# Performance work log

Hardware: AMD Instinct MI355X
Metric: run time of the kernel (lower is better)

The kernel has to match this reference:

```python
import jax, jax.numpy as jnp
import numpy as np

NUM_GROUPS = 32
EPS = 1e-5


def group_norm(x, w, b):
    # x: [B, C, H, W]
    B, C, H, W = x.shape
    g = x.reshape(B, NUM_GROUPS, C // NUM_GROUPS, H, W)
    mu = g.mean(axis=(2, 3, 4), keepdims=True)
    var = g.var(axis=(2, 3, 4), keepdims=True)
    g = (g - mu) * jax.lax.rsqrt(var + EPS)
    x = g.reshape(B, C, H, W)
    return x * w[None, :, None, None] + b[None, :, None, None]


def conv1x1(x, w, b):
    # 1x1 conv == channel matmul; x: [B, C, H, W], w: [O, C], b: [O]
    return jnp.einsum('bchw,oc->bohw', x, w) + b[None, :, None, None]


def setup_inputs() -> dict:
    key = jax.random.key(0)
    ks = jax.random.split(key, 11)
    C = 512
    B, H, W = 4, 64, 64
    s = 1.0 / np.sqrt(C)
    return {
        'x': jax.random.normal(ks[0], (B, C, H, W), jnp.float32),
        'gn_w': jax.random.uniform(ks[1], (C,), jnp.float32, 0.5, 1.5),
        'gn_b': jax.random.normal(ks[2], (C,), jnp.float32) * 0.1,
        'wq': jax.random.normal(ks[3], (C, C), jnp.float32) * s,
        'bq': jax.random.normal(ks[4], (C,), jnp.float32) * 0.01,
        'wk': jax.random.normal(ks[5], (C, C), jnp.float32) * s,
        'bk': jax.random.normal(ks[6], (C,), jnp.float32) * 0.01,
        'wv': jax.random.normal(ks[7], (C, C), jnp.float32) * s,
        'bv': jax.random.normal(ks[8], (C,), jnp.float32) * 0.01,
        'wo': jax.random.normal(ks[9], (C, C), jnp.float32) * s,
        'bo': jax.random.normal(ks[10], (C,), jnp.float32) * 0.01,
    }


def reference(x, gn_w, gn_b, wq, bq, wk, bk, wv, bv, wo, bo):
    B, C, H, W = x.shape
    h_ = group_norm(x, gn_w, gn_b)
    q = conv1x1(h_, wq, bq).reshape(B, C, H * W)   # [B, C, HW]
    k = conv1x1(h_, wk, bk).reshape(B, C, H * W)
    v = conv1x1(h_, wv, bv).reshape(B, C, H * W)
    # scores: q^T k, scaled by C^-0.5; softmax over keys
    scores = jnp.einsum('bci,bcj->bij', q, k) * (C ** -0.5)  # [B, HW, HW]
    attn = jax.nn.softmax(scores, axis=-1)
    # h_[b,c,i] = sum_j v[b,c,j] * attn[b,i,j]
    h_ = jnp.einsum('bcj,bij->bci', v, attn).reshape(B, C, H, W)
    return x + conv1x1(h_, wo, bo)
```

## Files before the change

### kernel.cpp

```cpp
#include <hip/hip_runtime.h>
#include <hip/hip_bf16.h>

typedef __attribute__((ext_vector_type(8))) __bf16 bf16x8;
typedef __attribute__((ext_vector_type(4))) float f32x4;

__device__ __forceinline__ unsigned short f2bf(float f) {
  union { float f; unsigned u; } v; v.f = f;
  unsigned r = v.u + 0x7fffu + ((v.u >> 16) & 1u);
  return (unsigned short)(r >> 16);
}

__device__ __forceinline__ void gload_lds16(const void* g, void* s) {
  __builtin_amdgcn_global_load_lds(
      (const __attribute__((address_space(1))) void*)g,
      (__attribute__((address_space(3))) void*)s, 16, 0, 0);
}

__global__ __launch_bounds__(256) void convert_w(
    const float* __restrict__ wq, const float* __restrict__ wk,
    const float* __restrict__ wv, const float* __restrict__ wo,
    unsigned short* __restrict__ dst, float* __restrict__ lrow) {
  if (blockIdx.x >= 4096) {
    lrow[((blockIdx.x - 4096) << 8) | threadIdx.x] = 0.f;
    return;
  }
  const int m = blockIdx.x >> 10;
  const float* src = (m == 0) ? wq : (m == 1) ? wk : (m == 2) ? wv : wo;
  const int idx = ((blockIdx.x & 1023) << 8) | threadIdx.x;
  dst[m * 262144 + idx] = f2bf(src[idx]);
}

__global__ __launch_bounds__(256) void zero_k(float* __restrict__ p, int n) {
  const int i = blockIdx.x * 256 + threadIdx.x;
  if (i < n) p[i] = 0.f;
}

__global__ __launch_bounds__(256) void gn_stats(
    const float* __restrict__ x, float2* __restrict__ partials) {
  const int bg = blockIdx.x >> 2, part = blockIdx.x & 3;
  const float* xg = x + (size_t)bg * 65536 + part * 1024;
  const int t = threadIdx.x;
  float s = 0.f, ss = 0.f;
#pragma unroll
  for (int r = 0; r < 16; ++r) {
    const float4 v = *(const float4*)(xg + (size_t)r * 4096 + t * 4);
    s += v.x + v.y + v.z + v.w;
    ss += v.x * v.x + v.y * v.y + v.z * v.z + v.w * v.w;
  }
#pragma unroll
  for (int m = 32; m; m >>= 1) { s += __shfl_xor(s, m); ss += __shfl_xor(ss, m); }
  __shared__ float red[8];
  const int wave = t >> 6, lane = t & 63;
  if (lane == 0) { red[wave] = s; red[wave + 4] = ss; }
  __syncthreads();
  if (t == 0) {
    float2 p;
    p.x = red[0] + red[1] + red[2] + red[3];
    p.y = red[4] + red[5] + red[6] + red[7];
    partials[blockIdx.x] = p;
  }
}

__global__ __launch_bounds__(256) void gn_apply(
    const float* __restrict__ x, const float2* __restrict__ partials,
    const float* __restrict__ gw, const float* __restrict__ gb,
    unsigned short* __restrict__ h_t) {
  const int bg = blockIdx.x >> 3, cc = blockIdx.x & 7;
  const int b = bg >> 5, g = bg & 31;
  const int t = threadIdx.x;
  __shared__ float chs[32];
  __shared__ unsigned short tile[16][520];
  if (t < 16) {
    const float2 p0 = partials[bg * 4 + 0], p1 = partials[bg * 4 + 1];
    const float2 p2 = partials[bg * 4 + 2], p3 = partials[bg * 4 + 3];
    const float S = p0.x + p1.x + p2.x + p3.x;
    const float SS = p0.y + p1.y + p2.y + p3.y;
    const float mu = S * (1.f / 65536.f);
    const float rstd = rsqrtf(SS * (1.f / 65536.f) - mu * mu + 1e-5f);
    const float sc = gw[g * 16 + t] * rstd;
    chs[t] = sc;
    chs[16 + t] = gb[g * 16 + t] - mu * sc;
  }
  __syncthreads();
  const float* xg = x + (size_t)bg * 65536 + cc * 512;
#pragma unroll
  for (int rr = 0; rr < 8; ++rr) {
    const int r = rr * 2 + (t >> 7), i = (t & 127) * 4;
    const float4 v = *(const float4*)(xg + (size_t)r * 4096 + i);
    const float sc = chs[r], sh = chs[16 + r];
    ushort4 o;
    o.x = f2bf(v.x * sc + sh); o.y = f2bf(v.y * sc + sh);
    o.z = f2bf(v.z * sc + sh); o.w = f2bf(v.w * sc + sh);
    *(ushort4*)&tile[r][i] = o;
  }
  __syncthreads();
  unsigned short* outp = h_t + ((size_t)b * 4096 + cc * 512) * 512 + g * 16;
#pragma unroll
  for (int rep = 0; rep < 4; ++rep) {
    const int task = rep * 256 + t;
    const int nl = task >> 1, half = (task & 1) * 8;
    ushort4 o0, o1;
    o0.x = tile[half + 0][nl]; o0.y = tile[half + 1][nl];
    o0.z = tile[half + 2][nl]; o0.w = tile[half + 3][nl];
    o1.x = tile[half + 4][nl]; o1.y = tile[half + 5][nl];
    o1.z = tile[half + 6][nl]; o1.w = tile[half + 7][nl];
    *(ushort4*)(outp + (size_t)nl * 512 + half) = o0;
    *(ushort4*)(outp + (size_t)nl * 512 + half + 4) = o1;
  }
}

__global__ __launch_bounds__(256) void reduce4_k(
    const float* __restrict__ part, const float* __restrict__ l,
    unsigned short* __restrict__ dst) {
  const size_t i = ((size_t)blockIdx.x * 256 + threadIdx.x) * 4;
  f32x4 s0 = *(const f32x4*)(part + i);
  f32x4 s1 = *(const f32x4*)(part + 2097152 + i);
  f32x4 s2 = *(const f32x4*)(part + 4194304 + i);
  f32x4 s3 = *(const f32x4*)(part + 6291456 + i);
  f32x4 s = (s0 + s1) + (s2 + s3);
  const float inv = 1.f / l[i >> 9];
  ushort4 o;
  o.x = f2bf(s[0] * inv); o.y = f2bf(s[1] * inv);
  o.z = f2bf(s[2] * inv); o.w = f2bf(s[3] * inv);
  *(ushort4*)(dst + i) = o;
}

__global__ __launch_bounds__(256) void gemm_qkv(
    const unsigned short* __restrict__ H, const unsigned short* __restrict__ W,
    unsigned short* __restrict__ q_t, unsigned short* __restrict__ k_t,
    unsigned short* __restrict__ v_ct,
    const float* __restrict__ bq, const float* __restrict__ bk,
    const float* __restrict__ bv, float qscale) {
  __shared__ __align__(16) char smem[49152];
  const int tid = threadIdx.x;
  const int wave = tid >> 6, lane = tid & 63;
  const int l15 = lane & 15, l4 = lane >> 4;
  const int wm = wave >> 1, wn = wave & 1;

  const int bx = blockIdx.x, by = blockIdx.y, bz = blockIdx.z;
  const int mode = bx >> 2;
  const int colv = (bx & 3) << 7;
  const int row0 = by << 7;
  const unsigned short* A = H + (size_t)bz * 2097152;
  const unsigned short* Bt = W + (size_t)bx * 65536;

  const int ar = tid >> 2;
  const int akc = (tid & 3) ^ ((tid >> 3) & 3);

  auto stage = [&](int kt, int bi) {
    const int kb = kt << 5;
    char* sAl = smem + bi * 16384 + wave * 1024;
    char* sBl = sAl + 8192;
    const unsigned short* gA = A + (size_t)(row0 + ar) * 512 + kb + akc * 8;
    const unsigned short* gB = Bt + (size_t)ar * 512 + kb + akc * 8;
    gload_lds16(gA, sAl);
    gload_lds16(gB, sBl);
    gload_lds16(gA + (size_t)64 * 512, sAl + 4096);
    gload_lds16(gB + (size_t)64 * 512, sBl + 4096);
  };

  f32x4 acc[4][4];
#pragma unroll
  for (int r = 0; r < 4; ++r)
#pragma unroll
    for (int c = 0; c < 4; ++c) acc[r][c] = (f32x4)0.f;

  const int xsw = (l4 ^ ((l15 >> 1) & 3)) << 4;

  auto compute = [&](int bi) {
    const char* pa = smem + bi * 16384 + (wm * 64 + l15) * 64 + xsw;
    const char* pb = smem + bi * 16384 + 8192 + (wn * 64 + l15) * 64 + xsw;
    bf16x8 af[4], bfr[4];
#pragma unroll
    for (int r = 0; r < 4; ++r) af[r] = *(const bf16x8*)(pa + r * 1024);
#pragma unroll
    for (int c = 0; c < 4; ++c) bfr[c] = *(const bf16x8*)(pb + c * 1024);
#pragma unroll
    for (int r = 0; r < 4; ++r)
#pragma unroll
      for (int c = 0; c < 4; ++c)
        acc[r][c] = __builtin_amdgcn_mfma_f32_16x16x32_bf16(af[r], bfr[c], acc[r][c], 0, 0, 0);
  };

  stage(0, 0);
  stage(1, 1);
  int bi = 0;
  for (int kt = 0; kt < 15; ++kt) {
    asm volatile("s_waitcnt vmcnt(4)" ::: "memory");
    __builtin_amdgcn_s_barrier();
    __builtin_amdgcn_sched_barrier(0);
    if (kt + 2 < 16) stage(kt + 2, (kt + 2) % 3);
    compute(bi);
    bi = (bi == 2) ? 0 : bi + 1;
  }
  asm volatile("s_waitcnt vmcnt(0)" ::: "memory");
  __builtin_amdgcn_s_barrier();
  __builtin_amdgcn_sched_barrier(0);
  compute(bi);

  const float* bias = (mode == 0) ? bq : (mode == 1) ? bk : bv;
  const float scale = (mode == 0) ? qscale : 1.0f;
  __syncthreads();
  if (mode < 2) {
    unsigned short* outp = ((mode == 0) ? q_t : k_t) + (size_t)bz * 2097152;
    unsigned short* tile = (unsigned short*)smem;
#pragma unroll
    for (int c = 0; c < 4; ++c) {
      const int coll = wn * 64 + c * 16 + l15;
      const float badd = bias[colv + coll];
#pragma unroll
      for (int r = 0; r < 4; ++r) {
        const int rowl = wm * 64 + r * 16 + l4 * 4;
#pragma unroll
        for (int j = 0; j < 4; ++j)
          tile[(rowl + j) * 136 + coll] = f2bf((acc[r][c][j] + badd) * scale);
      }
    }
    __syncthreads();
#pragma unroll
    for (int it = 0; it < 8; ++it) {
      const int idx = it * 256 + tid;
      const int rw = idx >> 4, ch = (idx & 15) * 8;
      const uint4 vv = *(const uint4*)&tile[rw * 136 + ch];
      *(uint4*)(outp + (size_t)(row0 + rw) * 512 + colv + ch) = vv;
    }
  } else {
    unsigned short* outp = v_ct + (size_t)bz * 2097152;
    unsigned short* tile = (unsigned short*)smem;
#pragma unroll
    for (int c = 0; c < 4; ++c) {
      const int coll = wn * 64 + c * 16 + l15;
      const float badd = bias[colv + coll];
#pragma unroll
      for (int r = 0; r < 4; ++r) {
        const int rowl = wm * 64 + r * 16 + l4 * 4;
#pragma unroll
        for (int j = 0; j < 4; ++j)
          tile[(rowl + j) * 132 + coll] = f2bf(acc[r][c][j] + badd);
      }
    }
    __syncthreads();
#pragma unroll 8
    for (int it = 0; it < 64; ++it) {
      const int idx = it * 256 + tid;
      const int cl = idx >> 7, il = idx & 127;
      outp[(size_t)(colv + cl) * 4096 + row0 + il] = tile[il * 132 + cl];
    }
  }
}

__global__ __launch_bounds__(512, 4) void gemm_s256(
    const unsigned short* __restrict__ A, const unsigned short* __restrict__ Bt,
    unsigned short* __restrict__ Out, float* __restrict__ lsum) {
  __shared__ __align__(16) char smem[73728];
  const int tid = threadIdx.x;
  const int wave = tid >> 6, lane = tid & 63;
  const int l15 = lane & 15, l4 = lane >> 4;
  const int wm = wave >> 1, wn = wave & 1;

  const int bz = blockIdx.z;
  A += (size_t)bz * 2097152;
  Bt += (size_t)bz * 2097152;
  Out += (size_t)bz * 16777216;
  lsum += (size_t)bz * 4096;

  const int id = blockIdx.y * 32 + blockIdx.x;
  const int xcd = id & 7, j = id >> 3;
  const int by = ((xcd >> 1) << 2) + (j >> 4);
  const int bx = ((xcd & 1) << 4) + (j & 15);
  const int row0 = by << 8, col0 = bx << 7;

  const int ar = tid >> 2;
  const int akc = (tid & 3) ^ ((tid >> 3) & 3);

  auto stage = [&](int kt, int bi) {
    const int kb = kt << 5;
    char* base = smem + bi * 24576;
    const unsigned short* gA = A + (size_t)(row0 + ar) * 512 + kb + akc * 8;
    const unsigned short* gB = Bt + (size_t)(col0 + ar) * 512 + kb + akc * 8;
    gload_lds16(gA, base + wave * 1024);
    gload_lds16(gA + (size_t)128 * 512, base + 8192 + wave * 1024);
    gload_lds16(gB, base + 16384 + wave * 1024);
  };

  f32x4 acc[4][4];
#pragma unroll
  for (int r = 0; r < 4; ++r)
#pragma unroll
    for (int c = 0; c < 4; ++c) acc[r][c] = (f32x4)0.f;

  const int xsw = (l4 ^ ((l15 >> 1) & 3)) << 4;

  auto compute = [&](int bi) {
    const char* pa = smem + bi * 24576 + (wm * 64 + l15) * 64 + xsw;
    const char* pb = smem + bi * 24576 + 16384 + (wn * 64 + l15) * 64 + xsw;
    bf16x8 af[4], bfr[4];
#pragma unroll
    for (int r = 0; r < 4; ++r) af[r] = *(const bf16x8*)(pa + r * 1024);
#pragma unroll
    for (int c = 0; c < 4; ++c) bfr[c] = *(const bf16x8*)(pb + c * 1024);
#pragma unroll
    for (int r = 0; r < 4; ++r)
#pragma unroll
      for (int c = 0; c < 4; ++c)
        acc[r][c] = __builtin_amdgcn_mfma_f32_16x16x32_bf16(af[r], bfr[c], acc[r][c], 0, 0, 0);
  };

  stage(0, 0);
  stage(1, 1);
  int bi = 0;
  for (int kt = 0; kt < 15; ++kt) {
    asm volatile("s_waitcnt vmcnt(3)" ::: "memory");
    __builtin_amdgcn_s_barrier();
    __builtin_amdgcn_sched_barrier(0);
    if (kt + 2 < 16) stage(kt + 2, (kt + 2) % 3);
    compute(bi);
    bi = (bi == 2) ? 0 : bi + 1;
  }
  asm volatile("s_waitcnt vmcnt(0)" ::: "memory");
  __builtin_amdgcn_s_barrier();
  __builtin_amdgcn_sched_barrier(0);
  compute(bi);

  __syncthreads();
  unsigned short* tile = (unsigned short*)smem;
#pragma unroll
  for (int c = 0; c < 4; ++c) {
    const int coll = wn * 64 + c * 16 + l15;
#pragma unroll
    for (int r = 0; r < 4; ++r) {
      const int rowl = wm * 64 + r * 16 + l4 * 4;
#pragma unroll
      for (int j = 0; j < 4; ++j)
        tile[(rowl + j) * 136 + coll] = f2bf(__expf(acc[r][c][j]));
    }
  }
  __syncthreads();
#pragma unroll
  for (int it = 0; it < 8; ++it) {
    const int idx = it * 512 + tid;
    const int rw = idx >> 4, ch = (idx & 15) * 8;
    const uint4 vv = *(const uint4*)&tile[rw * 136 + ch];
    *(uint4*)(Out + (size_t)(row0 + rw) * 4096 + col0 + ch) = vv;
    const unsigned* uu = (const unsigned*)&vv;
    float s = 0.f;
#pragma unroll
    for (int q = 0; q < 4; ++q) {
      union { unsigned u; float f; } w;
      w.u = uu[q] << 16; s += w.f;
      w.u = uu[q] & 0xffff0000u; s += w.f;
    }
    s += __shfl_xor(s, 1); s += __shfl_xor(s, 2);
    s += __shfl_xor(s, 4); s += __shfl_xor(s, 8);
    if ((lane & 15) == 0) atomicAdd(&lsum[row0 + rw], s);
  }
}

__global__ __launch_bounds__(512, 2) void gemm_pv(
    const unsigned short* __restrict__ P, const unsigned short* __restrict__ Vt,
    unsigned short* __restrict__ Out, const float* __restrict__ lrow) {
  __shared__ __align__(16) char smem[147456];
  const int tid = threadIdx.x;
  const int wave = tid >> 6, lane = tid & 63;
  const int l15 = lane & 15, l4 = lane >> 4;
  const int wm = wave >> 1, wn = wave & 1;

  const int L = blockIdx.x + ((blockIdx.y + (blockIdx.z << 4)) << 2);
  const int xcd = L & 7, j = L >> 3;
  const int panel = xcd * 8 + (j >> 2);
  const int bx = j & 3, by = panel & 15, bz = panel >> 4;
  const int row0 = by << 8, col0 = bx << 7;
  P += (size_t)bz * 16777216;
  Vt += (size_t)bz * 2097152;
  Out += (size_t)bz * 2097152;
  lrow += bz * 4096;

  const int sr = tid >> 3;
  const int sc8 = (tid & 7) ^ (sr & 7);
  const unsigned short* gA = P + (size_t)(row0 + sr) * 4096 + sc8 * 8;
  const unsigned short* gB = Vt + (size_t)(col0 + sr) * 4096 + sc8 * 8;

  auto stA = [&](int kt, int bi, int p) {
    gload_lds16(gA + (size_t)(p << 6) * 4096 + (kt << 6),
                smem + bi * 49152 + p * 8192 + wave * 1024);
  };
  auto stB = [&](int kt, int bi, int p) {
    gload_lds16(gB + (size_t)(p << 6) * 4096 + (kt << 6),
                smem + bi * 49152 + 32768 + p * 8192 + wave * 1024);
  };

  f32x4 acc[4][4];
#pragma unroll
  for (int r = 0; r < 4; ++r)
#pragma unroll
    for (int c = 0; c < 4; ++c) acc[r][c] = (f32x4)0.f;

  const int sw0 = (l4 ^ (l15 & 7)) << 4;
  const int sw1 = ((4 + l4) ^ (l15 & 7)) << 4;
  const int arow = (wm * 64 + l15) << 7;
  const int brow = (wn * 64 + l15) << 7;

  bf16x8 bfr[4][2];

  stA(0, 0, 0); stA(0, 0, 1); stA(0, 0, 2); stA(0, 0, 3);
  stB(0, 0, 0); stB(0, 0, 1);
  stA(1, 1, 0); stA(1, 1, 1); stA(1, 1, 2); stA(1, 1, 3);
  stB(1, 1, 0); stB(1, 1, 1);
  asm volatile("s_waitcnt vmcnt(6)" ::: "memory");
  __builtin_amdgcn_s_barrier();
  __builtin_amdgcn_sched_barrier(0);

  int bi = 0;
#pragma unroll 1
  for (int kt = 0; kt < 64; ++kt) {
    const char* bufA = smem + bi * 49152;
    const char* bufB = bufA + 32768;
    const int pb = (bi + 2) % 3;
    const bool pre = (kt + 2 < 64);
    bf16x8 a0, a1;
    a0 = *(const bf16x8*)(bufA + arow + sw0);
    a1 = *(const bf16x8*)(bufA + arow + sw1);
#pragma unroll
    for (int c = 0; c < 4; ++c) {
      bfr[c][0] = *(const bf16x8*)(bufB + brow + c * 2048 + sw0);
      bfr[c][1] = *(const bf16x8*)(bufB + brow + c * 2048 + sw1);
    }
    if (pre) { stA(kt + 2, pb, 0); stA(kt + 2, pb, 1); }
    __builtin_amdgcn_s_barrier();
    asm volatile("s_waitcnt lgkmcnt(0)" ::: "memory");
    __builtin_amdgcn_sched_barrier(0);
    __builtin_amdgcn_s_setprio(1);
#pragma unroll
    for (int c = 0; c < 4; ++c) {
      acc[0][c] = __builtin_amdgcn_mfma_f32_16x16x32_bf16(a0, bfr[c][0], acc[0][c], 0, 0, 0);
      acc[0][c] = __builtin_amdgcn_mfma_f32_16x16x32_bf16(a1, bfr[c][1], acc[0][c], 0, 0, 0);
    }
    __builtin_amdgcn_s_setprio(0);
    __builtin_amdgcn_s_barrier();
    a0 = *(const bf16x8*)(bufA + arow + 2048 + sw0);
    a1 = *(const bf16x8*)(bufA + arow + 2048 + sw1);
    if (pre) { stA(kt + 2, pb, 2); stA(kt + 2, pb, 3); }
    __builtin_amdgcn_s_barrier();
    asm volatile("s_waitcnt lgkmcnt(0)" ::: "memory");
    __builtin_amdgcn_sched_barrier(0);
    __builtin_amdgcn_s_setprio(1);
#pragma unroll
    for (int c = 0; c < 4; ++c) {
      acc[1][c] = __builtin_amdgcn_mfma_f32_16x16x32_bf16(a0, bfr[c][0], acc[1][c], 0, 0, 0);
      acc[1][c] = __builtin_amdgcn_mfma_f32_16x16x32_bf16(a1, bfr[c][1], acc[1][c], 0, 0, 0);
    }
    __builtin_amdgcn_s_setprio(0);
    __builtin_amdgcn_s_barrier();
    a0 = *(const bf16x8*)(bufA + arow + 4096 + sw0);
    a1 = *(const bf16x8*)(bufA + arow + 4096 + sw1);
    if (pre) { stB(kt + 2, pb, 0); stB(kt + 2, pb, 1); }
    __builtin_amdgcn_s_barrier();
    asm volatile("s_waitcnt lgkmcnt(0)" ::: "memory");
    __builtin_amdgcn_sched_barrier(0);
    __builtin_amdgcn_s_setprio(1);
#pragma unroll
    for (int c = 0; c < 4; ++c) {
      acc[2][c] = __builtin_amdgcn_mfma_f32_16x16x32_bf16(a0, bfr[c][0], acc[2][c], 0, 0, 0);
      acc[2][c] = __builtin_amdgcn_mfma_f32_16x16x32_bf16(a1, bfr[c][1], acc[2][c], 0, 0, 0);
    }
    __builtin_amdgcn_s_setprio(0);
    __builtin_amdgcn_s_barrier();
    a0 = *(const bf16x8*)(bufA + arow + 6144 + sw0);
    a1 = *(const bf16x8*)(bufA + arow + 6144 + sw1);
    __builtin_amdgcn_s_barrier();
    asm volatile("s_waitcnt lgkmcnt(0)" ::: "memory");
    __builtin_amdgcn_sched_barrier(0);
    __builtin_amdgcn_s_setprio(1);
#pragma unroll
    for (int c = 0; c < 4; ++c) {
      acc[3][c] = __builtin_amdgcn_mfma_f32_16x16x32_bf16(a0, bfr[c][0], acc[3][c], 0, 0, 0);
      acc[3][c] = __builtin_amdgcn_mfma_f32_16x16x32_bf16(a1, bfr[c][1], acc[3][c], 0, 0, 0);
    }
    __builtin_amdgcn_s_setprio(0);
    if (pre) asm volatile("s_waitcnt vmcnt(6)" ::: "memory");
    else     asm volatile("s_waitcnt vmcnt(0)" ::: "memory");
    __builtin_amdgcn_s_barrier();
    __builtin_amdgcn_sched_barrier(0);
    bi = (bi == 2) ? 0 : bi + 1;
  }

  __syncthreads();
  unsigned short* tile = (unsigned short*)smem;
#pragma unroll
  for (int c = 0; c < 4; ++c) {
    const int coll = wn * 64 + c * 16 + l15;
#pragma unroll
    for (int r = 0; r < 4; ++r) {
      const int rowl = wm * 64 + r * 16 + l4 * 4;
#pragma unroll
      for (int j = 0; j < 4; ++j) {
        const float v = acc[r][c][j] * (1.0f / lrow[row0 + rowl + j]);
        tile[(rowl + j) * 136 + coll] = f2bf(v);
      }
    }
  }
  __syncthreads();
#pragma unroll
  for (int it = 0; it < 8; ++it) {
    const int idx = it * 512 + tid;
    const int rw = idx >> 4, ch = (idx & 15) * 8;
    const uint4 vv = *(const uint4*)&tile[rw * 136 + ch];
    *(uint4*)(Out + (size_t)(row0 + rw) * 512 + col0 + ch) = vv;
  }
}

template <bool OUT_BF16, int BIAS_MODE, bool RESID, bool TRANS_OUT, int SWZ,
          bool COAL>
__global__ __launch_bounds__(256) void gemm_bt(
    const unsigned short* __restrict__ A, long long sA, int lda,
    const unsigned short* __restrict__ Bt, long long sB, int ldb,
    void* __restrict__ OutV, long long sO, int ldo,
    const float* __restrict__ bias,
    const float* __restrict__ resid, long long sR,
    int K, float scale) {
  __shared__ __align__(16) char smem[49152];
  const int tid = threadIdx.x;
  const int wave = tid >> 6, lane = tid & 63;
  const int l15 = lane & 15, l4 = lane >> 4;
  const int wm = wave >> 1, wn = wave & 1;

  int bx = blockIdx.x, by = blockIdx.y, bz = blockIdx.z;
  if constexpr (SWZ == 1) {
    const int id = by * 32 + bx;
    const int xcd = id & 7, j = id >> 3;
    by = ((xcd >> 1) << 3) + (j >> 4);
    bx = ((xcd & 1) << 4) + (j & 15);
  } else if constexpr (SWZ == 2) {
    const int L = bx + ((by + (bz << 5)) << 2);
    const int xcd = L & 7, j = L >> 3;
    const int pair = xcd * 16 + (j >> 2);
    bx = j & 3;
    by = pair & 31;
    bz = pair >> 5;
  }
  const int row0 = by << 7, col0 = bx << 7;
  A += (size_t)bz * sA;
  Bt += (size_t)bz * sB;
  if (RESID) resid += (size_t)bz * sR;
  if constexpr (BIAS_MODE == 3) bias += (size_t)bz * sR;
  char* outB = (char*)OutV + (size_t)bz * sO * (OUT_BF16 ? 2 : 4);

  const int ar = tid >> 2;
  const int akc = (tid & 3) ^ ((tid >> 3) & 3);

  auto stage = [&](int kt, int bi) {
    const int kb = kt << 5;
    char* sAl = smem + bi * 16384 + wave * 1024;
    char* sBl = sAl + 8192;
    const unsigned short* gA = A + (size_t)(row0 + ar) * lda + kb + akc * 8;
    const unsigned short* gB = Bt + (size_t)(col0 + ar) * ldb + kb + akc * 8;
    gload_lds16(gA, sAl);
    gload_lds16(gB, sBl);
    gload_lds16(gA + (size_t)64 * lda, sAl + 4096);
    gload_lds16(gB + (size_t)64 * ldb, sBl + 4096);
  };

  f32x4 acc[4][4];
#pragma unroll
  for (int r = 0; r < 4; ++r)
#pragma unroll
    for (int c = 0; c < 4; ++c) acc[r][c] = (f32x4)0.f;

  const int nk = K >> 5;
  const int xsw = (l4 ^ ((l15 >> 1) & 3)) << 4;

  auto compute = [&](int bi) {
    const char* pa = smem + bi * 16384 + (wm * 64 + l15) * 64 + xsw;
    const char* pb = smem + bi * 16384 + 8192 + (wn * 64 + l15) * 64 + xsw;
    bf16x8 af[4], bfr[4];
#pragma unroll
    for (int r = 0; r < 4; ++r) af[r] = *(const bf16x8*)(pa + r * 1024);
#pragma unroll
    for (int c = 0; c < 4; ++c) bfr[c] = *(const bf16x8*)(pb + c * 1024);
#pragma unroll
    for (int r = 0; r < 4; ++r)
#pragma unroll
      for (int c = 0; c < 4; ++c)
        acc[r][c] = __builtin_amdgcn_mfma_f32_16x16x32_bf16(af[r], bfr[c], acc[r][c], 0, 0, 0);
  };

  stage(0, 0);
  stage(1, 1);
  int bi = 0;
  for (int kt = 0; kt < nk - 1; ++kt) {
    asm volatile("s_waitcnt vmcnt(4)" ::: "memory");
    __builtin_amdgcn_s_barrier();
    __builtin_amdgcn_sched_barrier(0);
    if (kt + 2 < nk) stage(kt + 2, (kt + 2) % 3);
    compute(bi);
    bi = (bi == 2) ? 0 : bi + 1;
  }
  asm volatile("s_waitcnt vmcnt(0)" ::: "memory");
  __builtin_amdgcn_s_barrier();
  __builtin_amdgcn_sched_barrier(0);
  compute(bi);

  if constexpr (COAL && !TRANS_OUT) {
    __syncthreads();
    if constexpr (OUT_BF16) {
      unsigned short* tile = (unsigned short*)smem;
#pragma unroll
      for (int c = 0; c < 4; ++c) {
        const int coll = wn * 64 + c * 16 + l15;
        float badd = 0.f;
        if constexpr (BIAS_MODE == 1) badd = bias[col0 + coll];
#pragma unroll
        for (int r = 0; r < 4; ++r) {
          const int rowl = wm * 64 + r * 16 + l4 * 4;
#pragma unroll
          for (int j = 0; j < 4; ++j) {
            float v;
            if constexpr (BIAS_MODE == 3)
              v = acc[r][c][j] * (1.0f / bias[row0 + rowl + j]);
            else
              v = (acc[r][c][j] + badd) * scale;
            tile[(rowl + j) * 136 + coll] = f2bf(v);
          }
        }
      }
      __syncthreads();
      unsigned short* outp = (unsigned short*)outB;
#pragma unroll
      for (int it = 0; it < 8; ++it) {
        const int idx = it * 256 + tid;
        const int rw = idx >> 4, ch = (idx & 15) * 8;
        const uint4 vv = *(const uint4*)&tile[rw * 136 + ch];
        *(uint4*)(outp + (size_t)(row0 + rw) * ldo + col0 + ch) = vv;
      }
    } else {
      float* tile = (float*)smem;
#pragma unroll
      for (int p = 0; p < 2; ++p) {
        if (wm == p) {
#pragma unroll
          for (int c = 0; c < 4; ++c) {
            const int coll = wn * 64 + c * 16 + l15;
            float badd = 0.f;
            if constexpr (BIAS_MODE == 1) badd = bias[col0 + coll];
#pragma unroll
            for (int r = 0; r < 4; ++r) {
              const int rowl = r * 16 + l4 * 4;
#pragma unroll
              for (int j = 0; j < 4; ++j) {
                float v = acc[r][c][j] + badd;
                if constexpr (BIAS_MODE == 2) v += bias[row0 + p * 64 + rowl + j];
                tile[(rowl + j) * 132 + coll] = v * scale;
              }
            }
          }
        }
        __syncthreads();
        float* outp = (float*)outB;
#pragma unroll
        for (int it = 0; it < 8; ++it) {
          const int idx = it * 256 + tid;
          const int rw = idx >> 5, ch = (idx & 31) * 4;
          const int rowg = row0 + p * 64 + rw;
          f32x4 v = *(const f32x4*)&tile[rw * 132 + ch];
          if constexpr (RESID) {
            const float* rp = resid + (size_t)rowg * ldo + col0 + ch;
            v[0] += rp[0]; v[1] += rp[1]; v[2] += rp[2]; v[3] += rp[3];
          }
          *(f32x4*)(outp + (size_t)rowg * ldo + col0 + ch) = v;
        }
        __syncthreads();
      }
    }
  } else if constexpr (!TRANS_OUT) {
#pragma unroll
    for (int c = 0; c < 4; ++c) {
      const int colg = col0 + wn * 64 + c * 16 + l15;
      float badd = 0.f;
      if constexpr (BIAS_MODE == 1) badd = bias[colg];
#pragma unroll
      for (int r = 0; r < 4; ++r) {
        const int rowg = row0 + wm * 64 + r * 16 + l4 * 4;
#pragma unroll
        for (int j = 0; j < 4; ++j) {
          float v = acc[r][c][j] + badd;
          if constexpr (BIAS_MODE == 2) v += bias[rowg + j];
          v *= scale;
          if constexpr (RESID) v += resid[(size_t)(rowg + j) * ldo + colg];
          if constexpr (OUT_BF16)
            ((unsigned short*)outB)[(size_t)(rowg + j) * ldo + colg] = f2bf(v);
          else
            ((float*)outB)[(size_t)(rowg + j) * ldo + colg] = v;
        }
      }
    }
  } else {
    __syncthreads();
    unsigned short* tile = (unsigned short*)smem;
#pragma unroll
    for (int c = 0; c < 4; ++c) {
      const int coll = wn * 64 + c * 16 + l15;
      float badd = 0.f;
      if constexpr (BIAS_MODE == 1) badd = bias[col0 + coll];
#pragma unroll
      for (int r = 0; r < 4; ++r) {
        const int rowl = wm * 64 + r * 16 + l4 * 4;
#pragma unroll
        for (int j = 0; j < 4; ++j)
          tile[(rowl + j) * 132 + coll] = f2bf((acc[r][c][j] + badd) * scale);
      }
    }
    __syncthreads();
    unsigned short* outp = (unsigned short*)outB;
#pragma unroll 8
    for (int it = 0; it < 64; ++it) {
      const int idx = it * 256 + tid;
      const int cl = idx >> 7, il = idx & 127;
      outp[(size_t)(col0 + cl) * ldo + row0 + il] = tile[il * 132 + cl];
    }
  }
}

extern "C" void kernel_launch(void* const* d_in, const int* in_sizes, int n_in,
                              void* d_out, int out_size, void* d_ws, size_t ws_size,
                              hipStream_t stream) {
  const float* x   = (const float*)d_in[0];
  const float* gnw = (const float*)d_in[1];
  const float* gnb = (const float*)d_in[2];
  const float* wq  = (const float*)d_in[3];
  const float* bq  = (const float*)d_in[4];
  const float* wk  = (const float*)d_in[5];
  const float* bk  = (const float*)d_in[6];
  const float* wv  = (const float*)d_in[7];
  const float* bv  = (const float*)d_in[8];
  const float* wo  = (const float*)d_in[9];
  const float* bo  = (const float*)d_in[10];
  float* out = (float*)d_out;
  char* ws = (char*)d_ws;

  const size_t MB = 1u << 20;
  float2*         gnp  = (float2*)ws;
  float*          lrow = (float*)(ws + 64 * 1024);
  unsigned short* wbf  = (unsigned short*)(ws + 1 * MB);
  unsigned short* h_t  = (unsigned short*)(ws + 3 * MB);
  unsigned short* q_t  = (unsigned short*)(ws + 19 * MB);
  unsigned short* k_t  = (unsigned short*)(ws + 35 * MB);
  unsigned short* v_ct = (unsigned short*)(ws + 51 * MB);
  unsigned short* h2_t = (unsigned short*)(ws + 67 * MB);
  unsigned short* Pbuf = (unsigned short*)(ws + 83 * MB);
  float*          part = (float*)(ws + 115 * MB);

  const long long BS = 2097152;
  const float qscale = 0.044194173824159216f;
  const bool batched = ws_size >= 212 * MB;

  convert_w<<<dim3(4160), dim3(256), 0, stream>>>(wq, wk, wv, wo, wbf, lrow);
  gn_stats<<<dim3(512), dim3(256), 0, stream>>>(x, gnp);
  gn_apply<<<dim3(1024), dim3(256), 0, stream>>>(x, gnp, gnw, gnb, h_t);

  gemm_qkv<<<dim3(12, 32, 4), dim3(256), 0, stream>>>(
      h_t, wbf, q_t, k_t, v_ct, bq, bk, bv, qscale);

  if (batched) {
    gemm_s256<<<dim3(32, 16, 4), dim3(512), 0, stream>>>(q_t, k_t, Pbuf, lrow);
    gemm_pv<<<dim3(4, 16, 4), dim3(512), 0, stream>>>(Pbuf, v_ct, h2_t, lrow);
  } else {
    for (int b = 0; b < 4; ++b) {
      zero_k<<<dim3(16), dim3(256), 0, stream>>>(lrow, 4096);
      gemm_s256<<<dim3(32, 16, 1), dim3(512), 0, stream>>>(
          q_t + (size_t)b * BS, k_t + (size_t)b * BS, Pbuf, lrow);
      gemm_bt<false, 0, false, false, 0, true><<<dim3(4, 32, 4), 256, 0, stream>>>(
          Pbuf, 1024, 4096, v_ct + (size_t)b * BS, 1024, 4096,
          part, 2097152, 512, nullptr, nullptr, 0, 1024, 1.0f);
      reduce4_k<<<dim3(2048), dim3(256), 0, stream>>>(part, lrow, h2_t + (size_t)b * BS);
    }
  }

  gemm_bt<false, 2, true, false, 0, true><<<dim3(32, 4, 4), 256, 0, stream>>>(
      wbf + 786432, 0, 512, h2_t, BS, 512, out, BS, 4096, bo, x, BS, 512, 1.0f);
}
```

Before: 249.0 us.

## Enlarge QKV GEMM tile to 256 rows, fold GN stats into convert launch

The QKV projection GEMM now uses 512 threads and a 256-row by 128-column block tile. Each weight tile loaded into LDS is therefore reused across twice as many rows, and the grid has half as many blocks. The triple-buffered LDS staging grows to 72 KB, and the wait count drops to match the three loads issued per stage. The V transpose epilogue now writes 16-byte vectors instead of scalar shorts. Separately, the group-norm statistics blocks are appended to the weight-conversion kernel to save one launch, at the cost of higher LDS use and possibly lower occupancy in the GEMM.

```diff
diff --git a/kernel.cpp b/kernel.cpp
--- a/kernel.cpp
+++ b/kernel.cpp
@@ -19,46 +19,48 @@
 __global__ __launch_bounds__(256) void convert_w(
     const float* __restrict__ wq, const float* __restrict__ wk,
     const float* __restrict__ wv, const float* __restrict__ wo,
-    unsigned short* __restrict__ dst, float* __restrict__ lrow) {
-  if (blockIdx.x >= 4096) {
-    lrow[((blockIdx.x - 4096) << 8) | threadIdx.x] = 0.f;
+    unsigned short* __restrict__ dst, float* __restrict__ lrow,
+    const float* __restrict__ x, float2* __restrict__ partials) {
+  const int blk = blockIdx.x;
+  const int t = threadIdx.x;
+  if (blk >= 4160) {
+    const int bgq = blk - 4160;
+    const int bg = bgq >> 2, part = bgq & 3;
+    const float* xg = x + (size_t)bg * 65536 + part * 1024;
+    float s = 0.f, ss = 0.f;
+#pragma unroll
+    for (int r = 0; r < 16; ++r) {
+      const float4 v = *(const float4*)(xg + (size_t)r * 4096 + t * 4);
+      s += v.x + v.y + v.z + v.w;
+      ss += v.x * v.x + v.y * v.y + v.z * v.z + v.w * v.w;
+    }
+#pragma unroll
+    for (int m = 32; m; m >>= 1) { s += __shfl_xor(s, m); ss += __shfl_xor(ss, m); }
+    __shared__ float red[8];
+    const int wave = t >> 6, lane = t & 63;
+    if (lane == 0) { red[wave] = s; red[wave + 4] = ss; }
+    __syncthreads();
+    if (t == 0) {
+      float2 p;
+      p.x = red[0] + red[1] + red[2] + red[3];
+      p.y = red[4] + red[5] + red[6] + red[7];
+      partials[bgq] = p;
+    }
     return;
   }
-  const int m = blockIdx.x >> 10;
+  if (blk >= 4096) {
+    lrow[((blk - 4096) << 8) | t] = 0.f;
+    return;
+  }
+  const int m = blk >> 10;
   const float* src = (m == 0) ? wq : (m == 1) ? wk : (m == 2) ? wv : wo;
-  const int idx = ((blockIdx.x & 1023) << 8) | threadIdx.x;
+  const int idx = ((blk & 1023) << 8) | t;
   dst[m * 262144 + idx] = f2bf(src[idx]);
 }
 
 __global__ __launch_bounds__(256) void zero_k(float* __restrict__ p, int n) {
   const int i = blockIdx.x * 256 + threadIdx.x;
   if (i < n) p[i] = 0.f;
-}
-
-__global__ __launch_bounds__(256) void gn_stats(
-    const float* __restrict__ x, float2* __restrict__ partials) {
-  const int bg = blockIdx.x >> 2, part = blockIdx.x & 3;
-  const float* xg = x + (size_t)bg * 65536 + part * 1024;
-  const int t = threadIdx.x;
-  float s = 0.f, ss = 0.f;
-#pragma unroll
-  for (int r = 0; r < 16; ++r) {
-    const float4 v = *(const float4*)(xg + (size_t)r * 4096 + t * 4);
-    s += v.x + v.y + v.z + v.w;
-    ss += v.x * v.x + v.y * v.y + v.z * v.z + v.w * v.w;
-  }
-#pragma unroll
-  for (int m = 32; m; m >>= 1) { s += __shfl_xor(s, m); ss += __shfl_xor(ss, m); }
-  __shared__ float red[8];
-  const int wave = t >> 6, lane = t & 63;
-  if (lane == 0) { red[wave] = s; red[wave + 4] = ss; }
-  __syncthreads();
-  if (t == 0) {
-    float2 p;
-    p.x = red[0] + red[1] + red[2] + red[3];
-    p.y = red[4] + red[5] + red[6] + red[7];
-    partials[blockIdx.x] = p;
-  }
 }
 
 __global__ __launch_bounds__(256) void gn_apply(
@@ -125,13 +127,13 @@
   *(ushort4*)(dst + i) = o;
 }
 
-__global__ __launch_bounds__(256) void gemm_qkv(
+__global__ __launch_bounds__(512, 4) void gemm_qkv(
     const unsigned short* __restrict__ H, const unsigned short* __restrict__ W,
     unsigned short* __restrict__ q_t, unsigned short* __restrict__ k_t,
     unsigned short* __restrict__ v_ct,
     const float* __restrict__ bq, const float* __restrict__ bk,
     const float* __restrict__ bv, float qscale) {
-  __shared__ __align__(16) char smem[49152];
+  __shared__ __align__(16) char smem[73728];
   const int tid = threadIdx.x;
   const int wave = tid >> 6, lane = tid & 63;
   const int l15 = lane & 15, l4 = lane >> 4;
@@ -140,7 +142,7 @@
   const int bx = blockIdx.x, by = blockIdx.y, bz = blockIdx.z;
   const int mode = bx >> 2;
   const int colv = (bx & 3) << 7;
-  const int row0 = by << 7;
+  const int row0 = by << 8;
   const unsigned short* A = H + (size_t)bz * 2097152;
   const unsigned short* Bt = W + (size_t)bx * 65536;
 
@@ -149,14 +151,12 @@
 
   auto stage = [&](int kt, int bi) {
     const int kb = kt << 5;
-    char* sAl = smem + bi * 16384 + wave * 1024;
-    char* sBl = sAl + 8192;
+    char* base = smem + bi * 24576;
     const unsigned short* gA = A + (size_t)(row0 + ar) * 512 + kb + akc * 8;
     const unsigned short* gB = Bt + (size_t)ar * 512 + kb + akc * 8;
-    gload_lds16(gA, sAl);
-    gload_lds16(gB, sBl);
-    gload_lds16(gA + (size_t)64 * 512, sAl + 4096);
-    gload_lds16(gB + (size_t)64 * 512, sBl + 4096);
+    gload_lds16(gA, base + wave * 1024);
+    gload_lds16(gA + (size_t)128 * 512, base + 8192 + wave * 1024);
+    gload_lds16(gB, base + 16384 + wave * 1024);
   };
 
   f32x4 acc[4][4];
@@ -168,8 +168,8 @@
   const int xsw = (l4 ^ ((l15 >> 1) & 3)) << 4;
 
   auto compute = [&](int bi) {
-    const char* pa = smem + bi * 16384 + (wm * 64 + l15) * 64 + xsw;
-    const char* pb = smem + bi * 16384 + 8192 + (wn * 64 + l15) * 64 + xsw;
+    const char* pa = smem + bi * 24576 + (wm * 64 + l15) * 64 + xsw;
+    const char* pb = smem + bi * 24576 + 16384 + (wn * 64 + l15) * 64 + xsw;
     bf16x8 af[4], bfr[4];
 #pragma unroll
     for (int r = 0; r < 4; ++r) af[r] = *(const bf16x8*)(pa + r * 1024);
@@ -186,7 +186,7 @@
   stage(1, 1);
   int bi = 0;
   for (int kt = 0; kt < 15; ++kt) {
-    asm volatile("s_waitcnt vmcnt(4)" ::: "memory");
+    asm volatile("s_waitcnt vmcnt(3)" ::: "memory");
     __builtin_amdgcn_s_barrier();
     __builtin_amdgcn_sched_barrier(0);
     if (kt + 2 < 16) stage(kt + 2, (kt + 2) % 3);
@@ -219,7 +219,7 @@
     __syncthreads();
 #pragma unroll
     for (int it = 0; it < 8; ++it) {
-      const int idx = it * 256 + tid;
+      const int idx = it * 512 + tid;
       const int rw = idx >> 4, ch = (idx & 15) * 8;
       const uint4 vv = *(const uint4*)&tile[rw * 136 + ch];
       *(uint4*)(outp + (size_t)(row0 + rw) * 512 + colv + ch) = vv;
@@ -240,11 +240,14 @@
       }
     }
     __syncthreads();
-#pragma unroll 8
-    for (int it = 0; it < 64; ++it) {
-      const int idx = it * 256 + tid;
-      const int cl = idx >> 7, il = idx & 127;
-      outp[(size_t)(colv + cl) * 4096 + row0 + il] = tile[il * 132 + cl];
+#pragma unroll
+    for (int it = 0; it < 8; ++it) {
+      const int idx = it * 512 + tid;
+      const int cl = idx >> 5, ch8 = (idx & 31) * 8;
+      ushort ga[8];
+#pragma unroll
+      for (int q = 0; q < 8; ++q) ga[q] = tile[(ch8 + q) * 132 + cl];
+      *(uint4*)(outp + (size_t)(colv + cl) * 4096 + row0 + ch8) = *(const uint4*)ga;
     }
   }
 }
@@ -753,11 +756,10 @@
   const float qscale = 0.044194173824159216f;
   const bool batched = ws_size >= 212 * MB;
 
-  convert_w<<<dim3(4160), dim3(256), 0, stream>>>(wq, wk, wv, wo, wbf, lrow);
-  gn_stats<<<dim3(512), dim3(256), 0, stream>>>(x, gnp);
+  convert_w<<<dim3(4672), dim3(256), 0, stream>>>(wq, wk, wv, wo, wbf, lrow, x, gnp);
   gn_apply<<<dim3(1024), dim3(256), 0, stream>>>(x, gnp, gnw, gnb, h_t);
 
-  gemm_qkv<<<dim3(12, 32, 4), dim3(256), 0, stream>>>(
+  gemm_qkv<<<dim3(12, 16, 4), dim3(512), 0, stream>>>(
       h_t, wbf, q_t, k_t, v_ct, bq, bk, bv, qscale);
 
   if (batched) {
```

Result: slower. 256.7 us (+3.1%).
